# Optimization experiments

Hardware: AMD Instinct MI355X
Metric: run time of the kernel (lower is better)

The kernel has to match this reference:

```python
import jax, jax.numpy as jnp
import numpy as np

NUM_FUTURE = 4  # num_future_time_steps module constant


def _wmean(x, src, dst, ew, n):
    # Weighted mean aggregation over incoming edges (PyG SAGEConv aggr='mean'
    # with edge-weighted messages). x: [N,F] or [T,N,F].
    if x.ndim == 2:
        msg = x[src] * ew[:, None]                          # [E,F]
        agg = jax.ops.segment_sum(msg, dst, num_segments=n)  # [N,F]
    else:
        msg = x[:, src, :] * ew[None, :, None]              # [T,E,F]
        agg = jax.ops.segment_sum(jnp.moveaxis(msg, 1, 0), dst, num_segments=n)
        agg = jnp.moveaxis(agg, 0, 1)                       # [T,N,F]
    deg = jax.ops.segment_sum(jnp.ones_like(ew), dst, num_segments=n)
    return agg / jnp.clip(deg, 1.0)[:, None]


def _sage(x, src, dst, ew, Wr, Wroot, b, n):
    # WeightedSAGEConv: lin_rel(weighted-mean of neighbors) + lin_root(x)
    return _wmean(x, src, dst, ew, n) @ Wr + x @ Wroot + b


def _glstm(xseq, src, dst, ew, Wr, Wroot, b, h0, c0, n):
    # Graph LSTM: all four gates are WeightedSAGEConv([x_t, h]) ; the gate
    # convs share one gather/scatter (linear in agg), weights stacked to 4H.
    def step(carry, xt):
        h, c = carry
        inp = jnp.concatenate([xt, h], axis=-1)             # [N,2H]
        gates = _wmean(inp, src, dst, ew, n) @ Wr + inp @ Wroot + b  # [N,4H]
        i, f, g, o = jnp.split(gates, 4, axis=-1)
        c = jax.nn.sigmoid(f) * c + jax.nn.sigmoid(i) * jnp.tanh(g)
        h = jax.nn.sigmoid(o) * jnp.tanh(c)
        return (h, c), h
    (h, c), hs = jax.lax.scan(step, (h0, c0), xseq)
    return hs, c  # hs: [T,N,H]


def setup_inputs():
    T, N, E = 12, 20000, 400000
    F, H, O = 32, 64, 8
    key = jax.random.key(0)
    ks = jax.random.split(key, 12)
    nrm = lambda k, shp, fan: jax.random.normal(k, shp, dtype=jnp.float32) / np.float32(np.sqrt(fan))
    return {
        "x": jax.random.normal(ks[0], (T, N, F), dtype=jnp.float32),
        "edge_index": jax.random.randint(ks[1], (2, E), 0, N, dtype=jnp.int32),
        "edge_attr": jax.random.uniform(ks[2], (E,), dtype=jnp.float32),
        "sage_Wr": nrm(ks[3], (F, H), F),
        "sage_Wroot": nrm(ks[4], (F, H), F),
        "sage_b": jnp.zeros((H,), jnp.float32),
        "lstm1_Wr": nrm(ks[5], (2 * H, 4 * H), 2 * H),
        "lstm1_Wroot": nrm(ks[6], (2 * H, 4 * H), 2 * H),
        "lstm1_b": jnp.zeros((4 * H,), jnp.float32),
        "lstm2_Wr": nrm(ks[7], (2 * H, 4 * H), 2 * H),
        "lstm2_Wroot": nrm(ks[8], (2 * H, 4 * H), 2 * H),
        "lstm2_b": jnp.zeros((4 * H,), jnp.float32),
        "W_out": nrm(ks[9], (2 * H, O), 2 * H),
        "b_out": jnp.zeros((O,), jnp.float32),
    }


def reference(x, edge_index, edge_attr, sage_Wr, sage_Wroot, sage_b,
              lstm1_Wr, lstm1_Wroot, lstm1_b, lstm2_Wr, lstm2_Wroot, lstm2_b,
              W_out, b_out):
    src, dst = edge_index[0], edge_index[1]
    N = x.shape[1]
    H = sage_Wr.shape[1]
    emb = _sage(x, src, dst, edge_attr, sage_Wr, sage_Wroot, sage_b, N)  # [T,N,H]
    xr = jax.nn.relu(emb)  # dropout = identity (eval mode)
    h0 = jnp.zeros((N, H), x.dtype)
    c0 = jnp.zeros((N, H), x.dtype)
    h1, c1 = _glstm(xr, src, dst, edge_attr, lstm1_Wr, lstm1_Wroot, lstm1_b, h0, c0, N)
    h2, c2 = _glstm(xr, src, dst, edge_attr, lstm2_Wr, lstm2_Wroot, lstm2_b, h1[-1], c1, N)
    xs = jnp.concatenate([xr, h2], axis=-1)              # skip connection, [T,N,2H]
    out = xs[-NUM_FUTURE:] @ W_out + b_out               # [4,N,O]
    return out, c2, emb
```

## Files before the change

kernel.cpp:

```cpp
#include <hip/hip_runtime.h>
#include <math.h>

#define TT 12
#define FF 32
#define HH 64
#define OO 8
#define GG 256
#define NF 4
#define BR 16

typedef __bf16 bf16x8 __attribute__((ext_vector_type(8)));
typedef float  f32x4  __attribute__((ext_vector_type(4)));

__device__ __forceinline__ float sigmoidf_(float x){ return 1.f/(1.f+expf(-x)); }
__device__ __forceinline__ unsigned short f2bf(float f){
  unsigned int u = __float_as_uint(f);
  u += 0x7FFFu + ((u >> 16) & 1u);
  return (unsigned short)(u >> 16);
}
__device__ __forceinline__ float bf2f(unsigned short b){
  return __uint_as_float(((unsigned int)b) << 16);
}

__global__ void hist_kernel(const int* __restrict__ dst, int* __restrict__ cnt, int E){
  int e = blockIdx.x*blockDim.x + threadIdx.x;
  if (e < E) atomicAdd(&cnt[dst[e]], 1);
}

__global__ __launch_bounds__(1024) void scan_kernel(const int* __restrict__ cnt,
                                                    int* __restrict__ ptr,
                                                    float* __restrict__ invd, int N){
  __shared__ int buf[1024];
  __shared__ int carry;
  if (threadIdx.x == 0) carry = 0;
  __syncthreads();
  for (int base = 0; base < N; base += 1024){
    int i = base + threadIdx.x;
    int v = (i < N) ? cnt[i] : 0;
    buf[threadIdx.x] = v;
    __syncthreads();
    for (int off = 1; off < 1024; off <<= 1){
      int t = (threadIdx.x >= off) ? buf[threadIdx.x - off] : 0;
      __syncthreads();
      buf[threadIdx.x] += t;
      __syncthreads();
    }
    int incl = buf[threadIdx.x];
    if (i < N){
      ptr[i] = carry + incl - v;
      invd[i] = 1.f / fmaxf((float)v, 1.f);
    }
    __syncthreads();
    if (threadIdx.x == 1023){
      carry += incl;
      if (base + 1024 >= N) ptr[N] = carry;
    }
    __syncthreads();
  }
}

__global__ void fill_kernel(const int* __restrict__ src, const int* __restrict__ dst,
                            const float* __restrict__ ew, const int* __restrict__ ptr,
                            int* __restrict__ fill, int2* __restrict__ csr_sw, int E){
  int e = blockIdx.x*blockDim.x + threadIdx.x;
  if (e >= E) return;
  int d = dst[e];
  int pos = ptr[d] + atomicAdd(&fill[d], 1);
  int2 m; m.x = src[e]; m.y = __float_as_int(ew[e]);
  csr_sw[pos] = m;
}

__global__ void bf16_conv(const float* __restrict__ in, unsigned short* __restrict__ out, int n){
  int i = blockIdx.x*blockDim.x + threadIdx.x;
  if (i < n) out[i] = f2bf(in[i]);
}

__global__ void pack_wfrag(const float* __restrict__ Wr, const float* __restrict__ Wroot,
                           unsigned short* __restrict__ Wfrag){
  int idx = blockIdx.x*256 + threadIdx.x;
  if (idx >= 16*8*64*8) return;
  int e  = idx & 7;
  int l  = (idx >> 3) & 63;
  int ks = (idx >> 9) & 7;
  int jt = idx >> 12;
  int k = ks*32 + (l>>4)*8 + e;
  int j = jt*16 + (l&15);
  float v = (k < 128) ? Wr[(size_t)k*GG + j] : Wroot[(size_t)(k-128)*GG + j];
  Wfrag[idx] = f2bf(v);
}

__global__ void pack_sfrag(const float* __restrict__ Wr, const float* __restrict__ Wroot,
                           unsigned short* __restrict__ Sfrag){
  int idx = blockIdx.x*256 + threadIdx.x;
  if (idx >= 4*2*64*8) return;
  int e  = idx & 7;
  int l  = (idx >> 3) & 63;
  int ks = (idx >> 9) & 1;
  int jt = idx >> 10;
  int k = ks*32 + (l>>4)*8 + e;
  int j = jt*16 + (l&15);
  float v = (k < 32) ? Wr[(size_t)k*HH + j] : Wroot[(size_t)(k-32)*HH + j];
  Sfrag[idx] = f2bf(v);
}

__global__ __launch_bounds__(256) void sage_gather(
    const unsigned short* __restrict__ xb, const int* __restrict__ ptr,
    const int2* __restrict__ csr_sw,
    const float* __restrict__ invd, unsigned short* __restrict__ aggb, int N){
  int wave = threadIdx.x >> 6, lane = threadIdx.x & 63;
  int f = lane & 31, tp = lane >> 5;
  int n = blockIdx.x*4 + wave;
  if (n >= N) return;
  int beg = ptr[n], end = ptr[n+1];
  float id = invd[n];
  float acc[TT/2];
  #pragma unroll
  for (int th = 0; th < TT/2; ++th) acc[th] = 0.f;
  const size_t plane = (size_t)N*FF;
  int e = beg;
  for (; e+2 <= end; e += 2){
    int2 m0 = csr_sw[e], m1 = csr_sw[e+1];
    const unsigned short* p0 = xb + (size_t)m0.x*FF + f + (size_t)tp*plane;
    const unsigned short* p1 = xb + (size_t)m1.x*FF + f + (size_t)tp*plane;
    float w0 = __int_as_float(m0.y), w1 = __int_as_float(m1.y);
    #pragma unroll
    for (int th = 0; th < TT/2; ++th)
      acc[th] += bf2f(p0[2*th*plane])*w0 + bf2f(p1[2*th*plane])*w1;
  }
  for (; e < end; ++e){
    int2 m = csr_sw[e];
    const unsigned short* p = xb + (size_t)m.x*FF + f + (size_t)tp*plane;
    float wv = __int_as_float(m.y);
    #pragma unroll
    for (int th = 0; th < TT/2; ++th)
      acc[th] += bf2f(p[2*th*plane])*wv;
  }
  #pragma unroll
  for (int th = 0; th < TT/2; ++th)
    aggb[(size_t)(2*th+tp)*plane + (size_t)n*FF + f] = f2bf(acc[th] * id);
}

__global__ __launch_bounds__(256) void sage_mfma(
    const unsigned short* __restrict__ aggb, const unsigned short* __restrict__ xb,
    const unsigned short* __restrict__ Sfrag, const float* __restrict__ bias,
    float* __restrict__ emb, unsigned short* __restrict__ xrb, int Mrows){
  int tid = threadIdx.x, wave = tid >> 6, lane = tid & 63;
  int rbase = blockIdx.x*64 + wave*16;
  if (rbase >= Mrows) return;
  int l15 = lane & 15, l4 = lane >> 4;
  int row = rbase + l15;
  bf16x8 af0 = *(const bf16x8*)&aggb[(size_t)row*FF + l4*8];
  bf16x8 af1 = *(const bf16x8*)&xb  [(size_t)row*FF + l4*8];
  f32x4 acc[4];
  #pragma unroll
  for (int jt = 0; jt < 4; ++jt){
    float bv = bias[jt*16 + l15];
    acc[jt][0]=bv; acc[jt][1]=bv; acc[jt][2]=bv; acc[jt][3]=bv;
  }
  #pragma unroll
  for (int jt = 0; jt < 4; ++jt){
    bf16x8 b0 = *(const bf16x8*)&Sfrag[(size_t)(((jt*2+0)*64) + lane) * 8];
    bf16x8 b1 = *(const bf16x8*)&Sfrag[(size_t)(((jt*2+1)*64) + lane) * 8];
    acc[jt] = __builtin_amdgcn_mfma_f32_16x16x32_bf16(af0, b0, acc[jt], 0, 0, 0);
    acc[jt] = __builtin_amdgcn_mfma_f32_16x16x32_bf16(af1, b1, acc[jt], 0, 0, 0);
  }
  #pragma unroll
  for (int jt = 0; jt < 4; ++jt){
    int col = jt*16 + l15;
    #pragma unroll
    for (int i = 0; i < 4; ++i){
      int ro = rbase + l4*4 + i;
      float v = acc[jt][i];
      emb[(size_t)ro*HH + col] = v;
      xrb[(size_t)ro*HH + col] = f2bf(fmaxf(v, 0.f));
    }
  }
}

__global__ __launch_bounds__(256) void xr_gather(
    const unsigned short* __restrict__ xrb, const int* __restrict__ ptr,
    const int2* __restrict__ csr_sw,
    const float* __restrict__ invd, unsigned short* __restrict__ xr_aggb, int N){
  int wave = threadIdx.x >> 6, lane = threadIdx.x & 63;
  int n = blockIdx.x*4 + wave;
  if (n >= N) return;
  int beg = ptr[n], end = ptr[n+1];
  float id = invd[n];
  float acc[TT];
  #pragma unroll
  for (int t = 0; t < TT; ++t) acc[t] = 0.f;
  const size_t plane = (size_t)N*HH;
  int e = beg;
  for (; e+2 <= end; e += 2){
    int2 m0 = csr_sw[e], m1 = csr_sw[e+1];
    const unsigned short* p0 = xrb + (size_t)m0.x*HH + lane;
    const unsigned short* p1 = xrb + (size_t)m1.x*HH + lane;
    float w0 = __int_as_float(m0.y), w1 = __int_as_float(m1.y);
    #pragma unroll
    for (int t = 0; t < TT; ++t)
      acc[t] += bf2f(p0[t*plane])*w0 + bf2f(p1[t*plane])*w1;
  }
  for (; e < end; ++e){
    int2 m = csr_sw[e];
    const unsigned short* p = xrb + (size_t)m.x*HH + lane;
    float wv = __int_as_float(m.y);
    #pragma unroll
    for (int t = 0; t < TT; ++t)
      acc[t] += bf2f(p[t*plane])*wv;
  }
  #pragma unroll
  for (int t = 0; t < TT; ++t)
    xr_aggb[(size_t)t*plane + (size_t)n*HH + lane] = f2bf(acc[t] * id);
}

__global__ __launch_bounds__(256) void lstm_mfma(
    const unsigned short* __restrict__ xrb_t, const unsigned short* __restrict__ xraggb_t,
    const unsigned short* __restrict__ h_prev, unsigned short* __restrict__ h_next,
    float* __restrict__ c, const float* __restrict__ invd,
    const int* __restrict__ ptr, const int2* __restrict__ csr_sw,
    const unsigned short* __restrict__ Wfrag, const float* __restrict__ bias,
    unsigned short* __restrict__ h2_store, int N){
  __shared__ __align__(16) unsigned short Albuf[BR][264];
  __shared__ float gbuf[BR][260];
  int tid = threadIdx.x, wave = tid >> 6, lane = tid & 63;
  int base = blockIdx.x * BR;

  for (int r4 = 0; r4 < 4; ++r4){
    int r = wave*4 + r4;
    int n = base + r;
    if (n < N){
      float id = invd[n];
      int beg = ptr[n], end = ptr[n+1];
      float a0=0.f,a1=0.f,a2=0.f,a3=0.f,a4=0.f,a5=0.f,a6=0.f,a7=0.f;
      int e = beg;
      for (; e+8 <= end; e += 8){
        int2 m0=csr_sw[e+0], m1=csr_sw[e+1], m2=csr_sw[e+2], m3=csr_sw[e+3];
        int2 m4=csr_sw[e+4], m5=csr_sw[e+5], m6=csr_sw[e+6], m7=csr_sw[e+7];
        a0 += bf2f(h_prev[(size_t)m0.x*HH+lane])*__int_as_float(m0.y);
        a1 += bf2f(h_prev[(size_t)m1.x*HH+lane])*__int_as_float(m1.y);
        a2 += bf2f(h_prev[(size_t)m2.x*HH+lane])*__int_as_float(m2.y);
        a3 += bf2f(h_prev[(size_t)m3.x*HH+lane])*__int_as_float(m3.y);
        a4 += bf2f(h_prev[(size_t)m4.x*HH+lane])*__int_as_float(m4.y);
        a5 += bf2f(h_prev[(size_t)m5.x*HH+lane])*__int_as_float(m5.y);
        a6 += bf2f(h_prev[(size_t)m6.x*HH+lane])*__int_as_float(m6.y);
        a7 += bf2f(h_prev[(size_t)m7.x*HH+lane])*__int_as_float(m7.y);
      }
      for (; e < end; ++e){
        int2 m = csr_sw[e];
        a0 += bf2f(h_prev[(size_t)m.x*HH+lane])*__int_as_float(m.y);
      }
      float hag = (((a0+a1)+(a2+a3))+((a4+a5)+(a6+a7))) * id;
      Albuf[r][    lane] = xraggb_t[(size_t)n*HH + lane];
      Albuf[r][ 64+lane] = f2bf(hag);
      Albuf[r][128+lane] = xrb_t [(size_t)n*HH + lane];
      Albuf[r][192+lane] = h_prev[(size_t)n*HH + lane];
    } else {
      Albuf[r][lane] = Albuf[r][64+lane] = Albuf[r][128+lane] = Albuf[r][192+lane] = 0;
    }
  }
  __syncthreads();

  int l15 = lane & 15, l4 = lane >> 4;
  f32x4 acc[4];
  #pragma unroll
  for (int jtl = 0; jtl < 4; ++jtl){
    float bv = bias[wave*64 + jtl*16 + l15];
    acc[jtl][0]=bv; acc[jtl][1]=bv; acc[jtl][2]=bv; acc[jtl][3]=bv;
  }
  #pragma unroll
  for (int ks = 0; ks < 8; ++ks){
    bf16x8 af = *(const bf16x8*)&Albuf[l15][ks*32 + l4*8];
    #pragma unroll
    for (int jtl = 0; jtl < 4; ++jtl){
      int jt = wave*4 + jtl;
      bf16x8 bf = *(const bf16x8*)&Wfrag[(size_t)(((jt*8 + ks)*64) + lane) * 8];
      acc[jtl] = __builtin_amdgcn_mfma_f32_16x16x32_bf16(af, bf, acc[jtl], 0, 0, 0);
    }
  }
  #pragma unroll
  for (int jtl = 0; jtl < 4; ++jtl){
    int col = wave*64 + jtl*16 + l15;
    #pragma unroll
    for (int i = 0; i < 4; ++i)
      gbuf[l4*4 + i][col] = acc[jtl][i];
  }
  __syncthreads();

  for (int r = wave; r < BR; r += 4){
    int n = base + r;
    if (n >= N) continue;
    float gi = gbuf[r][lane], gf = gbuf[r][64+lane], gg2 = gbuf[r][128+lane], go = gbuf[r][192+lane];
    float cn = sigmoidf_(gf)*c[(size_t)n*HH+lane] + sigmoidf_(gi)*tanhf(gg2);
    float hn = sigmoidf_(go)*tanhf(cn);
    c[(size_t)n*HH+lane] = cn;
    unsigned short hb = f2bf(hn);
    h_next[(size_t)n*HH+lane] = hb;
    if (h2_store) h2_store[(size_t)n*HH+lane] = hb;
  }
}

__global__ void out_gemm(const unsigned short* __restrict__ xr8, const unsigned short* __restrict__ h2s,
                         const float* __restrict__ Wout, const float* __restrict__ bout,
                         float* __restrict__ out, int N){
  int idx = blockIdx.x*blockDim.x + threadIdx.x;
  if (idx >= NF*N*OO) return;
  int o = idx & (OO-1);
  int row = idx >> 3;
  const unsigned short* xv = xr8 + (size_t)row*HH;
  const unsigned short* hv = h2s + (size_t)row*HH;
  float acc = bout[o];
  #pragma unroll
  for (int k = 0; k < HH; ++k)
    acc += bf2f(xv[k])*Wout[k*OO+o] + bf2f(hv[k])*Wout[(HH+k)*OO+o];
  out[idx] = acc;
}

__global__ void copyk(const float* __restrict__ s, float* __restrict__ d, int n){
  int i = blockIdx.x*blockDim.x + threadIdx.x;
  if (i < n) d[i] = s[i];
}

extern "C" void kernel_launch(void* const* d_in, const int* in_sizes, int n_in,
                              void* d_out, int out_size, void* d_ws, size_t ws_size,
                              hipStream_t stream){
  const float* x      = (const float*)d_in[0];
  const int*   ei     = (const int*)  d_in[1];
  const float* ew     = (const float*)d_in[2];
  const float* sWr    = (const float*)d_in[3];
  const float* sWroot = (const float*)d_in[4];
  const float* sb     = (const float*)d_in[5];
  const float* l1Wr   = (const float*)d_in[6];
  const float* l1Wroot= (const float*)d_in[7];
  const float* l1b    = (const float*)d_in[8];
  const float* l2Wr   = (const float*)d_in[9];
  const float* l2Wroot= (const float*)d_in[10];
  const float* l2b    = (const float*)d_in[11];
  const float* Wout   = (const float*)d_in[12];
  const float* bout   = (const float*)d_in[13];

  const int E = in_sizes[2];
  const int N = in_sizes[0] / (TT*FF);
  const int* src = ei;
  const int* dst = ei + E;

  float* out0   = (float*)d_out;
  float* c2out  = out0 + (size_t)NF*N*OO;
  float* embout = c2out + (size_t)N*HH;

  float* w = (float*)d_ws;
  float* cbuf   = w;  w += (size_t)N*HH;
  float* invd   = w;  w += N;
  int*   cnt    = (int*)w;  w += N;
  int*   fill   = (int*)w;  w += N;
  int*   ptr    = (int*)w;  w += (N+2);
  int2*  csr_sw = (int2*)w; w += (size_t)2*E;
  unsigned short* Wf1 = (unsigned short*)w; w += (size_t)16*8*64*8/2;
  unsigned short* Wf2 = (unsigned short*)w; w += (size_t)16*8*64*8/2;
  unsigned short* Sfg = (unsigned short*)w; w += (size_t)4*2*64*8/2;
  unsigned short* xb     = (unsigned short*)w; w += (size_t)TT*N*FF/2;
  unsigned short* aggb   = (unsigned short*)w; w += (size_t)TT*N*FF/2;
  unsigned short* xrb    = (unsigned short*)w; w += (size_t)TT*N*HH/2;
  unsigned short* xraggb = (unsigned short*)w; w += (size_t)TT*N*HH/2;
  unsigned short* hA     = (unsigned short*)w; w += (size_t)N*HH/2;
  unsigned short* hB     = (unsigned short*)w; w += (size_t)N*HH/2;
  unsigned short* h2s    = (unsigned short*)w; w += (size_t)NF*N*HH/2;

  hipMemsetAsync(cnt,  0, (size_t)N*4, stream);
  hipMemsetAsync(fill, 0, (size_t)N*4, stream);
  hipMemsetAsync(hA,   0, (size_t)N*HH*2, stream);
  hipMemsetAsync(cbuf, 0, (size_t)N*HH*4, stream);

  hist_kernel<<<(E+255)/256, 256, 0, stream>>>(dst, cnt, E);
  scan_kernel<<<1, 1024, 0, stream>>>(cnt, ptr, invd, N);
  fill_kernel<<<(E+255)/256, 256, 0, stream>>>(src, dst, ew, ptr, fill, csr_sw, E);

  pack_wfrag<<<(16*8*64*8+255)/256, 256, 0, stream>>>(l1Wr, l1Wroot, Wf1);
  pack_wfrag<<<(16*8*64*8+255)/256, 256, 0, stream>>>(l2Wr, l2Wroot, Wf2);
  pack_sfrag<<<(4*2*64*8+255)/256, 256, 0, stream>>>(sWr, sWroot, Sfg);
  bf16_conv<<<((size_t)TT*N*FF+255)/256, 256, 0, stream>>>(x, xb, TT*N*FF);

  sage_gather<<<(N+3)/4, 256, 0, stream>>>(xb, ptr, csr_sw, invd, aggb, N);
  {
    int Mrows = TT*N;
    sage_mfma<<<(Mrows+63)/64, 256, 0, stream>>>(aggb, xb, Sfg, sb, embout, xrb, Mrows);
  }
  xr_gather<<<(N+3)/4, 256, 0, stream>>>(xrb, ptr, csr_sw, invd, xraggb, N);

  const int sBlocks = (N+BR-1)/BR;
  unsigned short* hp = hA; unsigned short* hn = hB;
  for (int t = 0; t < TT; ++t){
    lstm_mfma<<<sBlocks, 256, 0, stream>>>(xrb + (size_t)t*N*HH, xraggb + (size_t)t*N*HH,
                                           hp, hn, cbuf, invd, ptr, csr_sw,
                                           Wf1, l1b, nullptr, N);
    unsigned short* tmp = hp; hp = hn; hn = tmp;
  }
  for (int t = 0; t < TT; ++t){
    unsigned short* store = (t >= TT-NF) ? (h2s + (size_t)(t-(TT-NF))*N*HH) : nullptr;
    lstm_mfma<<<sBlocks, 256, 0, stream>>>(xrb + (size_t)t*N*HH, xraggb + (size_t)t*N*HH,
                                           hp, hn, cbuf, invd, ptr, csr_sw,
                                           Wf2, l2b, store, N);
    unsigned short* tmp = hp; hp = hn; hn = tmp;
  }

  out_gemm<<<((size_t)NF*N*OO+255)/256, 256, 0, stream>>>(xrb + (size_t)(TT-NF)*N*HH, h2s,
                                                          Wout, bout, out0, N);
  copyk<<<((size_t)N*HH+255)/256, 256, 0, stream>>>(cbuf, c2out, N*HH);
}
```

Measured before the change: 1.143 ms.

## Use one wave per node in LSTM step kernel and unroll gathers by four

Measured after the change: 1.115 ms. 2.5% less time.

```diff
diff --git a/kernel.cpp b/kernel.cpp
--- a/kernel.cpp
+++ b/kernel.cpp
@@ -118,14 +118,18 @@
   for (int th = 0; th < TT/2; ++th) acc[th] = 0.f;
   const size_t plane = (size_t)N*FF;
   int e = beg;
-  for (; e+2 <= end; e += 2){
-    int2 m0 = csr_sw[e], m1 = csr_sw[e+1];
+  for (; e+4 <= end; e += 4){
+    int2 m0 = csr_sw[e], m1 = csr_sw[e+1], m2 = csr_sw[e+2], m3 = csr_sw[e+3];
     const unsigned short* p0 = xb + (size_t)m0.x*FF + f + (size_t)tp*plane;
     const unsigned short* p1 = xb + (size_t)m1.x*FF + f + (size_t)tp*plane;
+    const unsigned short* p2 = xb + (size_t)m2.x*FF + f + (size_t)tp*plane;
+    const unsigned short* p3 = xb + (size_t)m3.x*FF + f + (size_t)tp*plane;
     float w0 = __int_as_float(m0.y), w1 = __int_as_float(m1.y);
+    float w2 = __int_as_float(m2.y), w3 = __int_as_float(m3.y);
     #pragma unroll
     for (int th = 0; th < TT/2; ++th)
-      acc[th] += bf2f(p0[2*th*plane])*w0 + bf2f(p1[2*th*plane])*w1;
+      acc[th] += bf2f(p0[2*th*plane])*w0 + bf2f(p1[2*th*plane])*w1
+               + bf2f(p2[2*th*plane])*w2 + bf2f(p3[2*th*plane])*w3;
   }
   for (; e < end; ++e){
     int2 m = csr_sw[e];
@@ -191,14 +195,18 @@
   for (int t = 0; t < TT; ++t) acc[t] = 0.f;
   const size_t plane = (size_t)N*HH;
   int e = beg;
-  for (; e+2 <= end; e += 2){
-    int2 m0 = csr_sw[e], m1 = csr_sw[e+1];
+  for (; e+4 <= end; e += 4){
+    int2 m0 = csr_sw[e], m1 = csr_sw[e+1], m2 = csr_sw[e+2], m3 = csr_sw[e+3];
     const unsigned short* p0 = xrb + (size_t)m0.x*HH + lane;
     const unsigned short* p1 = xrb + (size_t)m1.x*HH + lane;
+    const unsigned short* p2 = xrb + (size_t)m2.x*HH + lane;
+    const unsigned short* p3 = xrb + (size_t)m3.x*HH + lane;
     float w0 = __int_as_float(m0.y), w1 = __int_as_float(m1.y);
+    float w2 = __int_as_float(m2.y), w3 = __int_as_float(m3.y);
     #pragma unroll
     for (int t = 0; t < TT; ++t)
-      acc[t] += bf2f(p0[t*plane])*w0 + bf2f(p1[t*plane])*w1;
+      acc[t] += bf2f(p0[t*plane])*w0 + bf2f(p1[t*plane])*w1
+              + bf2f(p2[t*plane])*w2 + bf2f(p3[t*plane])*w3;
   }
   for (; e < end; ++e){
     int2 m = csr_sw[e];
@@ -213,7 +221,7 @@
     xr_aggb[(size_t)t*plane + (size_t)n*HH + lane] = f2bf(acc[t] * id);
 }
 
-__global__ __launch_bounds__(256) void lstm_mfma(
+__global__ __launch_bounds__(1024) void lstm_mfma(
     const unsigned short* __restrict__ xrb_t, const unsigned short* __restrict__ xraggb_t,
     const unsigned short* __restrict__ h_prev, unsigned short* __restrict__ h_next,
     float* __restrict__ c, const float* __restrict__ invd,
@@ -224,71 +232,62 @@
   __shared__ float gbuf[BR][260];
   int tid = threadIdx.x, wave = tid >> 6, lane = tid & 63;
   int base = blockIdx.x * BR;
-
-  for (int r4 = 0; r4 < 4; ++r4){
-    int r = wave*4 + r4;
-    int n = base + r;
-    if (n < N){
-      float id = invd[n];
-      int beg = ptr[n], end = ptr[n+1];
-      float a0=0.f,a1=0.f,a2=0.f,a3=0.f,a4=0.f,a5=0.f,a6=0.f,a7=0.f;
-      int e = beg;
-      for (; e+8 <= end; e += 8){
-        int2 m0=csr_sw[e+0], m1=csr_sw[e+1], m2=csr_sw[e+2], m3=csr_sw[e+3];
-        int2 m4=csr_sw[e+4], m5=csr_sw[e+5], m6=csr_sw[e+6], m7=csr_sw[e+7];
-        a0 += bf2f(h_prev[(size_t)m0.x*HH+lane])*__int_as_float(m0.y);
-        a1 += bf2f(h_prev[(size_t)m1.x*HH+lane])*__int_as_float(m1.y);
-        a2 += bf2f(h_prev[(size_t)m2.x*HH+lane])*__int_as_float(m2.y);
-        a3 += bf2f(h_prev[(size_t)m3.x*HH+lane])*__int_as_float(m3.y);
-        a4 += bf2f(h_prev[(size_t)m4.x*HH+lane])*__int_as_float(m4.y);
-        a5 += bf2f(h_prev[(size_t)m5.x*HH+lane])*__int_as_float(m5.y);
-        a6 += bf2f(h_prev[(size_t)m6.x*HH+lane])*__int_as_float(m6.y);
-        a7 += bf2f(h_prev[(size_t)m7.x*HH+lane])*__int_as_float(m7.y);
-      }
-      for (; e < end; ++e){
-        int2 m = csr_sw[e];
-        a0 += bf2f(h_prev[(size_t)m.x*HH+lane])*__int_as_float(m.y);
-      }
-      float hag = (((a0+a1)+(a2+a3))+((a4+a5)+(a6+a7))) * id;
-      Albuf[r][    lane] = xraggb_t[(size_t)n*HH + lane];
-      Albuf[r][ 64+lane] = f2bf(hag);
-      Albuf[r][128+lane] = xrb_t [(size_t)n*HH + lane];
-      Albuf[r][192+lane] = h_prev[(size_t)n*HH + lane];
-    } else {
-      Albuf[r][lane] = Albuf[r][64+lane] = Albuf[r][128+lane] = Albuf[r][192+lane] = 0;
-    }
+  int n = base + wave;
+
+  if (n < N){
+    float id = invd[n];
+    int beg = ptr[n], end = ptr[n+1];
+    float a0=0.f,a1=0.f,a2=0.f,a3=0.f,a4=0.f,a5=0.f,a6=0.f,a7=0.f;
+    int e = beg;
+    for (; e+8 <= end; e += 8){
+      int2 m0=csr_sw[e+0], m1=csr_sw[e+1], m2=csr_sw[e+2], m3=csr_sw[e+3];
+      int2 m4=csr_sw[e+4], m5=csr_sw[e+5], m6=csr_sw[e+6], m7=csr_sw[e+7];
+      a0 += bf2f(h_prev[(size_t)m0.x*HH+lane])*__int_as_float(m0.y);
+      a1 += bf2f(h_prev[(size_t)m1.x*HH+lane])*__int_as_float(m1.y);
+      a2 += bf2f(h_prev[(size_t)m2.x*HH+lane])*__int_as_float(m2.y);
+      a3 += bf2f(h_prev[(size_t)m3.x*HH+lane])*__int_as_float(m3.y);
+      a4 += bf2f(h_prev[(size_t)m4.x*HH+lane])*__int_as_float(m4.y);
+      a5 += bf2f(h_prev[(size_t)m5.x*HH+lane])*__int_as_float(m5.y);
+      a6 += bf2f(h_prev[(size_t)m6.x*HH+lane])*__int_as_float(m6.y);
+      a7 += bf2f(h_prev[(size_t)m7.x*HH+lane])*__int_as_float(m7.y);
+    }
+    for (; e < end; ++e){
+      int2 m = csr_sw[e];
+      a0 += bf2f(h_prev[(size_t)m.x*HH+lane])*__int_as_float(m.y);
+    }
+    float hag = (((a0+a1)+(a2+a3))+((a4+a5)+(a6+a7))) * id;
+    Albuf[wave][    lane] = xraggb_t[(size_t)n*HH + lane];
+    Albuf[wave][ 64+lane] = f2bf(hag);
+    Albuf[wave][128+lane] = xrb_t [(size_t)n*HH + lane];
+    Albuf[wave][192+lane] = h_prev[(size_t)n*HH + lane];
+  } else {
+    Albuf[wave][lane] = Albuf[wave][64+lane] = Albuf[wave][128+lane] = Albuf[wave][192+lane] = 0;
   }
   __syncthreads();
 
   int l15 = lane & 15, l4 = lane >> 4;
-  f32x4 acc[4];
-  #pragma unroll
-  for (int jtl = 0; jtl < 4; ++jtl){
-    float bv = bias[wave*64 + jtl*16 + l15];
-    acc[jtl][0]=bv; acc[jtl][1]=bv; acc[jtl][2]=bv; acc[jtl][3]=bv;
+  int jt = wave;
+  f32x4 acc;
+  {
+    float bv = bias[jt*16 + l15];
+    acc[0]=bv; acc[1]=bv; acc[2]=bv; acc[3]=bv;
   }
   #pragma unroll
   for (int ks = 0; ks < 8; ++ks){
     bf16x8 af = *(const bf16x8*)&Albuf[l15][ks*32 + l4*8];
-    #pragma unroll
-    for (int jtl = 0; jtl < 4; ++jtl){
-      int jt = wave*4 + jtl;
-      bf16x8 bf = *(const bf16x8*)&Wfrag[(size_t)(((jt*8 + ks)*64) + lane) * 8];
-      acc[jtl] = __builtin_amdgcn_mfma_f32_16x16x32_bf16(af, bf, acc[jtl], 0, 0, 0);
-    }
-  }
-  #pragma unroll
-  for (int jtl = 0; jtl < 4; ++jtl){
-    int col = wave*64 + jtl*16 + l15;
+    bf16x8 bf = *(const bf16x8*)&Wfrag[(size_t)(((jt*8 + ks)*64) + lane) * 8];
+    acc = __builtin_amdgcn_mfma_f32_16x16x32_bf16(af, bf, acc, 0, 0, 0);
+  }
+  {
+    int col = jt*16 + l15;
     #pragma unroll
     for (int i = 0; i < 4; ++i)
-      gbuf[l4*4 + i][col] = acc[jtl][i];
+      gbuf[l4*4 + i][col] = acc[i];
   }
   __syncthreads();
 
-  for (int r = wave; r < BR; r += 4){
-    int n = base + r;
-    if (n >= N) continue;
+  if (n < N){
+    int r = wave;
     float gi = gbuf[r][lane], gf = gbuf[r][64+lane], gg2 = gbuf[r][128+lane], go = gbuf[r][192+lane];
     float cn = sigmoidf_(gf)*c[(size_t)n*HH+lane] + sigmoidf_(gi)*tanhf(gg2);
     float hn = sigmoidf_(go)*tanhf(cn);
@@ -389,16 +388,16 @@
   const int sBlocks = (N+BR-1)/BR;
   unsigned short* hp = hA; unsigned short* hn = hB;
   for (int t = 0; t < TT; ++t){
-    lstm_mfma<<<sBlocks, 256, 0, stream>>>(xrb + (size_t)t*N*HH, xraggb + (size_t)t*N*HH,
-                                           hp, hn, cbuf, invd, ptr, csr_sw,
-                                           Wf1, l1b, nullptr, N);
+    lstm_mfma<<<sBlocks, 1024, 0, stream>>>(xrb + (size_t)t*N*HH, xraggb + (size_t)t*N*HH,
+                                            hp, hn, cbuf, invd, ptr, csr_sw,
+                                            Wf1, l1b, nullptr, N);
     unsigned short* tmp = hp; hp = hn; hn = tmp;
   }
   for (int t = 0; t < TT; ++t){
     unsigned short* store = (t >= TT-NF) ? (h2s + (size_t)(t-(TT-NF))*N*HH) : nullptr;
-    lstm_mfma<<<sBlocks, 256, 0, stream>>>(xrb + (size_t)t*N*HH, xraggb + (size_t)t*N*HH,
-                                           hp, hn, cbuf, invd, ptr, csr_sw,
-                                           Wf2, l2b, store, N);
+    lstm_mfma<<<sBlocks, 1024, 0, stream>>>(xrb + (size_t)t*N*HH, xraggb + (size_t)t*N*HH,
+                                            hp, hn, cbuf, invd, ptr, csr_sw,
+                                            Wf2, l2b, store, N);
     unsigned short* tmp = hp; hp = hn; hn = tmp;
   }
 
```
